# Kernel tuning notes

Hardware: AMD Instinct MI355X
Metric: run time of the kernel (lower is better)

Reference implementation:

```python
import jax, jax.numpy as jnp
import numpy as np

D_MODEL = 1024

def setup_inputs() -> dict:
    key = jax.random.key(0)
    k1, k2 = jax.random.split(key, 2)
    x = jax.random.normal(k1, (4, 2048, D_MODEL), dtype=jnp.float32)
    W_attn = jax.random.normal(k2, (3 * D_MODEL, D_MODEL), dtype=jnp.float32) * (1.0 / np.sqrt(D_MODEL))
    b_attn = jnp.zeros((3 * D_MODEL,), dtype=jnp.float32)
    return {"x": x, "W_attn": W_attn, "b_attn": b_attn}

def reference(x, W_attn, b_attn):
    B, T, C = x.shape
    # fused QKV projection; torch split order is (k, q, v)
    kqv = x @ W_attn.T + b_attn            # [B, T, 3C]
    k, q, v = jnp.split(kqv, 3, axis=-1)   # each [B, T, C]
    # NOTE: original computes k @ q^T (quirk), scaled by sqrt(d_model)
    scores = jnp.einsum('btc,bsc->bts', k, q) / jnp.sqrt(jnp.asarray(C, x.dtype))
    causal = jnp.tril(jnp.ones((T, T), dtype=bool))
    scores = jnp.where(causal[None, :, :], scores, -jnp.inf)
    attn = jax.nn.softmax(scores, axis=-1)
    return jnp.einsum('bts,bsc->btc', attn, v)
```

## Files before the change

kernel.cpp:

```cpp
#include <hip/hip_runtime.h>

typedef __bf16 bf16x8 __attribute__((ext_vector_type(8)));
typedef float f32x4 __attribute__((ext_vector_type(4)));
typedef float fl4 __attribute__((ext_vector_type(4)));
typedef unsigned short us4 __attribute__((ext_vector_type(4)));
typedef unsigned short us8 __attribute__((ext_vector_type(8)));

__device__ __forceinline__ unsigned short f2bf(float f) {
  unsigned u = __builtin_bit_cast(unsigned, f);
  u += 0x7fffu + ((u >> 16) & 1u);
  return (unsigned short)(u >> 16);
}
__device__ __forceinline__ float bf2f(unsigned short h) {
  unsigned u = ((unsigned)h) << 16;
  return __builtin_bit_cast(float, u);
}

__device__ __forceinline__ void async16(const void* g, void* l) {
  __builtin_amdgcn_global_load_lds(
      (const __attribute__((address_space(1))) unsigned int*)g,
      (__attribute__((address_space(3))) unsigned int*)l, 16, 0, 0);
}

#define BARM() asm volatile("s_barrier" ::: "memory")
#define VMCNT4() asm volatile("s_waitcnt vmcnt(4)" ::: "memory")
#define LGKM0() asm volatile("s_waitcnt lgkmcnt(0)" ::: "memory")
#define LGKM8() asm volatile("s_waitcnt lgkmcnt(8)" ::: "memory")
#define SCHEDB() __builtin_amdgcn_sched_barrier(0)

__global__ __launch_bounds__(256) void cvt_bf16_2(const float* __restrict__ sA,
                                                  unsigned short* __restrict__ dA, int nA,
                                                  const float* __restrict__ sB,
                                                  unsigned short* __restrict__ dB, int nB) {
  int i = blockIdx.x * 256 + threadIdx.x;
  const float* s;
  unsigned short* d;
  if (i < nA) {
    s = sA; d = dA;
  } else {
    i -= nA;
    if (i >= nB) return;
    s = sB; d = dB;
  }
  fl4 f = ((const fl4*)s)[i];
  us4 o;
  o[0] = f2bf(f[0]); o[1] = f2bf(f[1]); o[2] = f2bf(f[2]); o[3] = f2bf(f[3]);
  ((us4*)d)[i] = o;
}

__global__ __launch_bounds__(256) void transpose_v(const unsigned short* __restrict__ kqv,
                                                   unsigned short* __restrict__ vT) {
  int b = blockIdx.z;
  int t0 = blockIdx.x * 64;
  int c0 = blockIdx.y * 64;
  __shared__ unsigned short tile[64][68];
  int tid = threadIdx.x;
#pragma unroll
  for (int i = 0; i < 4; ++i) {
    int idx = i * 256 + tid;
    int r = idx >> 4;
    int c4 = (idx & 15) * 4;
    const unsigned short* src = kqv + ((size_t)(b * 2048 + t0 + r)) * 3072 + 2048 + c0 + c4;
    us4 v = *(const us4*)src;
    *(us4*)&tile[r][c4] = v;
  }
  __syncthreads();
#pragma unroll
  for (int i = 0; i < 4; ++i) {
    int idx = i * 256 + tid;
    int rc = idx >> 4;
    int t4 = (idx & 15) * 4;
    us4 v;
    v[0] = tile[t4 + 0][rc]; v[1] = tile[t4 + 1][rc];
    v[2] = tile[t4 + 2][rc]; v[3] = tile[t4 + 3][rc];
    unsigned short* dst = vT + ((size_t)(b * 1024 + c0 + rc)) * 2048 + t0 + t4;
    *(us4*)dst = v;
  }
}

template <int EPI>
__global__ __launch_bounds__(512, 2) void gemm8p(
    const unsigned short* __restrict__ A, int lda, long long sA,
    const unsigned short* __restrict__ B, int ldb, long long sB,
    void* __restrict__ Cv, int ldc, long long sC,
    const float* __restrict__ bias, float scale, int K, int NBX) {
  int bx, by;
  const int bz = blockIdx.z;
  if (EPI == 0) {
    int flat = blockIdx.x;
    int q = (int)gridDim.x >> 3;
    int swz = (flat & 7) * q + (flat >> 3);
    bx = swz % NBX; by = swz / NBX;
  } else {
    bx = blockIdx.x; by = blockIdx.y;
    if (EPI == 1 && bx > by) return;
  }
  A += (size_t)bz * sA;
  B += (size_t)bz * sB;
  const int rowBase = by * 256;
  const int colBase = bx * 256;
  const int nk = (EPI == 2) ? (rowBase + 256) / 64 : K / 64;

  __shared__ __align__(16) unsigned char lds[131072];
  const int tid = threadIdx.x;
  const int lane = tid & 63;
  const int wid = tid >> 6;
  const int wr = wid >> 2;
  const int wc = wid & 3;
  const int l15 = lane & 15, l4 = lane >> 4, l7 = lane & 7;

  f32x4 acc[8][4] = {};
  bf16x8 af0[4][2], af1[4][2], bf0[2][2], bf1[2][2];

  const unsigned short* Ab = A + (size_t)rowBase * lda;
  const unsigned short* Bb = B + (size_t)colBase * ldb;
  unsigned loff[2][2];
  unsigned lldso[2];
#pragma unroll
  for (int i = 0; i < 2; ++i) {
    int off = (i * 512 + tid) * 16;
    int r = off >> 7;
    int sb = ((off >> 4) & 7) ^ (r & 7);
    lldso[i] = (unsigned)off;
#pragma unroll
    for (int h = 0; h < 2; ++h)
      loff[h][i] = (unsigned)((h * 128 + r) * lda + sb * 8);
  }

  auto STAGE = [&](int bufc, int isB, int half, const unsigned short* Gb, int koff) {
#pragma unroll
    for (int i = 0; i < 2; ++i)
      async16(Gb + (size_t)(loff[half][i] + (unsigned)koff),
              lds + bufc * 65536 + isB * 32768 + half * 16384 + lldso[i]);
  };
  auto RDA = [&](int bufc, int m, int kk) -> bf16x8 {
    int row = m * 16 + l15;
    int blk = (kk * 4 + l4) ^ l7;
    return *(const bf16x8*)(lds + bufc * 65536 + wr * 16384 + row * 128 + blk * 16);
  };
  auto RDB = [&](int bufc, int n, int kk) -> bf16x8 {
    int row = (wc & 1) * 64 + n * 16 + l15;
    int blk = (kk * 4 + l4) ^ l7;
    return *(const bf16x8*)(lds + bufc * 65536 + 32768 + (wc >> 1) * 16384 +
                            row * 128 + blk * 16);
  };

#define RDA8(dst, BUF, Q)                                                      \
  _Pragma("unroll") for (int mi = 0; mi < 4; ++mi)                             \
  _Pragma("unroll") for (int kk = 0; kk < 2; ++kk)                             \
      dst[mi][kk] = RDA((BUF), (Q) * 4 + mi, kk)
#define RDB4(dst, BUF, NB)                                                     \
  _Pragma("unroll") for (int nj = 0; nj < 2; ++nj)                             \
  _Pragma("unroll") for (int kk = 0; kk < 2; ++kk)                             \
      dst[nj][kk] = RDB((BUF), (NB) + nj, kk)

#define MFMAQ(MB, NB, AF, BF)                                                  \
  _Pragma("unroll") for (int kk = 0; kk < 2; ++kk)                             \
  _Pragma("unroll") for (int mi = 0; mi < 4; ++mi)                             \
  _Pragma("unroll") for (int nj = 0; nj < 2; ++nj)                             \
      acc[(MB) + mi][(NB) + nj] = __builtin_amdgcn_mfma_f32_16x16x32_bf16(     \
          AF[mi][kk], BF[nj][kk], acc[(MB) + mi][(NB) + nj], 0, 0, 0)

#define PH(RDS, STG, HINT, GATE, MB, NB, AF, BF)                               \
  do {                                                                         \
    RDS;                                                                       \
    STG;                                                                       \
    HINT;                                                                      \
    BARM();                                                                    \
    LGKM0();                                                                   \
    SCHEDB();                                                                  \
    __builtin_amdgcn_s_setprio(1);                                             \
    MFMAQ(MB, NB, AF, BF);                                                     \
    __builtin_amdgcn_s_setprio(0);                                             \
    GATE;                                                                      \
    BARM();                                                                    \
  } while (0)

  STAGE(0, 0, 0, Ab, 0);
  STAGE(0, 0, 1, Ab, 0);
  STAGE(0, 1, 0, Bb, 0);
  STAGE(0, 1, 1, Bb, 0);
  STAGE(1, 1, 0, Bb, 64);
  STAGE(1, 1, 1, Bb, 64);
  VMCNT4();
  BARM();

  const int nt2 = nk >> 1;
  for (int it = 0; it < nt2; ++it) {
    int t = it * 2;
    int kA1 = (t + 1) * 64;
    int k2 = (t + 2 < nk - 1 ? t + 2 : nk - 1) * 64;
    int k3 = (t + 3 < nk - 1 ? t + 3 : nk - 1) * 64;
    PH({ RDA8(af0, 0, 0); RDB4(bf0, 0, 0); }, STAGE(1, 0, 0, Ab, kA1), LGKM8(),
       (void)0, 0, 0, af0, bf0);
    PH({ RDB4(bf1, 0, 2); }, STAGE(1, 0, 1, Ab, kA1), (void)0,
       (void)0, 0, 2, af0, bf1);
    PH({ RDA8(af1, 0, 1); }, STAGE(0, 1, 0, Bb, k2), (void)0,
       (void)0, 4, 2, af1, bf1);
    PH({}, STAGE(0, 1, 1, Bb, k2), (void)0,
       VMCNT4(), 4, 0, af1, bf0);
    PH({ RDA8(af0, 1, 0); RDB4(bf0, 1, 0); }, STAGE(0, 0, 0, Ab, k2), LGKM8(),
       (void)0, 0, 0, af0, bf0);
    PH({ RDB4(bf1, 1, 2); }, STAGE(0, 0, 1, Ab, k2), (void)0,
       (void)0, 0, 2, af0, bf1);
    PH({ RDA8(af1, 1, 1); }, STAGE(1, 1, 0, Bb, k3), (void)0,
       (void)0, 4, 2, af1, bf1);
    PH({}, STAGE(1, 1, 1, Bb, k3), (void)0,
       VMCNT4(), 4, 0, af1, bf0);
  }
#undef PH
#undef MFMAQ
#undef RDA8
#undef RDB4

  const int cr = l4 * 4;
  if constexpr (EPI == 0) {
    unsigned short* C = (unsigned short*)Cv;
#pragma unroll
    for (int n = 0; n < 4; ++n) {
      int col = colBase + wc * 64 + n * 16 + l15;
      float bv = bias[col];
#pragma unroll
      for (int m = 0; m < 8; ++m) {
        int row = rowBase + wr * 128 + m * 16 + cr;
#pragma unroll
        for (int i = 0; i < 4; ++i)
          C[(size_t)(row + i) * ldc + col] = f2bf(acc[m][n][i] + bv);
      }
    }
  } else if constexpr (EPI == 1) {
    unsigned short* C = (unsigned short*)Cv + (size_t)bz * sC;
#pragma unroll
    for (int n = 0; n < 4; ++n) {
      int col = colBase + wc * 64 + n * 16 + l15;
#pragma unroll
      for (int m = 0; m < 8; ++m) {
        int row = rowBase + wr * 128 + m * 16 + cr;
#pragma unroll
        for (int i = 0; i < 4; ++i)
          C[(size_t)(row + i) * ldc + col] = f2bf(acc[m][n][i] * scale);
      }
    }
  } else {
    float* C = (float*)Cv + (size_t)bz * sC;
#pragma unroll
    for (int n = 0; n < 4; ++n) {
      int col = colBase + wc * 64 + n * 16 + l15;
#pragma unroll
      for (int m = 0; m < 8; ++m) {
        int row = rowBase + wr * 128 + m * 16 + cr;
#pragma unroll
        for (int i = 0; i < 4; ++i)
          C[(size_t)(row + i) * ldc + col] = acc[m][n][i];
      }
    }
  }
}

__global__ __launch_bounds__(256) void softmax_causal(unsigned short* __restrict__ S) {
  const int T = 2048;
  int t = blockIdx.x, b = blockIdx.y;
  unsigned short* row = S + ((size_t)b * T + t) * T;
  const int nv = t + 1;
  const int bound = ((t >> 8) + 1) << 8;
  int tid = threadIdx.x;
  int lane = tid & 63, wid = tid >> 6;
  int s0 = tid * 8;
  us8 raw = {};
  if (s0 < nv) raw = *(const us8*)(row + s0);
  float v[8];
  float m = -3.0e38f;
#pragma unroll
  for (int j = 0; j < 8; ++j) {
    v[j] = bf2f(raw[j]);
    if (s0 + j < nv) m = fmaxf(m, v[j]);
  }
#pragma unroll
  for (int o = 32; o > 0; o >>= 1) m = fmaxf(m, __shfl_xor(m, o, 64));
  __shared__ float red[4];
  if (lane == 0) red[wid] = m;
  __syncthreads();
  m = fmaxf(fmaxf(red[0], red[1]), fmaxf(red[2], red[3]));
  __syncthreads();
  float sum = 0.f;
#pragma unroll
  for (int j = 0; j < 8; ++j) {
    float e = (s0 + j < nv) ? exp2f(v[j] - m) : 0.f;
    v[j] = e;
    sum += e;
  }
#pragma unroll
  for (int o = 32; o > 0; o >>= 1) sum += __shfl_xor(sum, o, 64);
  if (lane == 0) red[wid] = sum;
  __syncthreads();
  sum = red[0] + red[1] + red[2] + red[3];
  float inv = 1.0f / sum;
  if (s0 < bound) {
    us8 outv;
#pragma unroll
    for (int j = 0; j < 8; ++j) outv[j] = f2bf(v[j] * inv);
    *(us8*)(row + s0) = outv;
  }
}

extern "C" void kernel_launch(void* const* d_in, const int* in_sizes, int n_in,
                              void* d_out, int out_size, void* d_ws, size_t ws_size,
                              hipStream_t stream) {
  const float* x = (const float*)d_in[0];
  const float* W = (const float*)d_in[1];
  const float* bias = (const float*)d_in[2];
  float* out = (float*)d_out;

  char* ws = (char*)d_ws;
  if (ws_size < 106954752u) return;
  unsigned short* xbf = (unsigned short*)(ws);
  unsigned short* vT = xbf;
  unsigned short* wbf = (unsigned short*)(ws + 16777216);
  unsigned short* kqv = (unsigned short*)(ws + 23068672);
  unsigned short* S = (unsigned short*)(ws + 73400320);

  const float kSoftmaxScale = 1.4426950408889634f / 32.0f;

  cvt_bf16_2<<<11264, 256, 0, stream>>>(x, xbf, 2097152, W, wbf, 786432);

  gemm8p<0><<<dim3(384, 1, 1), 512, 0, stream>>>(
      xbf, 1024, 0LL, wbf, 1024, 0LL, kqv, 3072, 0LL, bias, 1.0f, 1024, 12);

  transpose_v<<<dim3(32, 16, 4), 256, 0, stream>>>(kqv, vT);

  gemm8p<1><<<dim3(8, 8, 4), 512, 0, stream>>>(
      kqv, 3072, 2048LL * 3072, kqv + 1024, 3072, 2048LL * 3072,
      S, 2048, 2048LL * 2048, nullptr, kSoftmaxScale, 1024, 0);

  softmax_causal<<<dim3(2048, 4), 256, 0, stream>>>(S);

  gemm8p<2><<<dim3(4, 8, 4), 512, 0, stream>>>(
      S, 2048, 2048LL * 2048, vT, 2048, 1024LL * 2048,
      out, 1024, 2048LL * 1024, nullptr, 1.0f, 2048, 0);
}
```

Measured before the change: 189.6 us.

## Fuse causal softmax into PV GEMM with online-softmax kernel; change LDS swizzle

Replaces the separate softmax pass and the PV GEMM with one flash-style kernel. It reads the bf16 scaled scores, keeps a running max and sum per row, rescales the accumulators, and multiplies by V with MFMA. This removes a full read-modify-write of the score matrix and one launch. In exchange it uses a small 128x128 tile with a K step of 32 and barriers every step, which may leave the MFMA units poorly fed. The GEMM LDS swizzle is also changed from a per-row XOR to a simpler XOR on bit 2 of the row, which may change bank conflicts.

After: 265.5 us. 1.4x slower.

```diff
diff --git a/kernel.cpp b/kernel.cpp
--- a/kernel.cpp
+++ b/kernel.cpp
@@ -99,7 +99,7 @@
   B += (size_t)bz * sB;
   const int rowBase = by * 256;
   const int colBase = bx * 256;
-  const int nk = (EPI == 2) ? (rowBase + 256) / 64 : K / 64;
+  const int nk = K / 64;
 
   __shared__ __align__(16) unsigned char lds[131072];
   const int tid = threadIdx.x;
@@ -107,7 +107,7 @@
   const int wid = tid >> 6;
   const int wr = wid >> 2;
   const int wc = wid & 3;
-  const int l15 = lane & 15, l4 = lane >> 4, l7 = lane & 7;
+  const int l15 = lane & 15, l4 = lane >> 4;
 
   f32x4 acc[8][4] = {};
   bf16x8 af0[4][2], af1[4][2], bf0[2][2], bf1[2][2];
@@ -120,11 +120,12 @@
   for (int i = 0; i < 2; ++i) {
     int off = (i * 512 + tid) * 16;
     int r = off >> 7;
-    int sb = ((off >> 4) & 7) ^ (r & 7);
+    int c = off & 127;
+    int cs = c ^ (((r >> 2) & 1) << 5);
     lldso[i] = (unsigned)off;
 #pragma unroll
     for (int h = 0; h < 2; ++h)
-      loff[h][i] = (unsigned)((h * 128 + r) * lda + sb * 8);
+      loff[h][i] = (unsigned)((h * 128 + r) * lda + (cs >> 1));
   }
 
   auto STAGE = [&](int bufc, int isB, int half, const unsigned short* Gb, int koff) {
@@ -135,14 +136,14 @@
   };
   auto RDA = [&](int bufc, int m, int kk) -> bf16x8 {
     int row = m * 16 + l15;
-    int blk = (kk * 4 + l4) ^ l7;
-    return *(const bf16x8*)(lds + bufc * 65536 + wr * 16384 + row * 128 + blk * 16);
+    int cs = ((kk * 4 + l4) * 16) ^ (((row >> 2) & 1) << 5);
+    return *(const bf16x8*)(lds + bufc * 65536 + wr * 16384 + row * 128 + cs);
   };
   auto RDB = [&](int bufc, int n, int kk) -> bf16x8 {
     int row = (wc & 1) * 64 + n * 16 + l15;
-    int blk = (kk * 4 + l4) ^ l7;
+    int cs = ((kk * 4 + l4) * 16) ^ (((row >> 2) & 1) << 5);
     return *(const bf16x8*)(lds + bufc * 65536 + 32768 + (wc >> 1) * 16384 +
-                            row * 128 + blk * 16);
+                            row * 128 + cs);
   };
 
 #define RDA8(dst, BUF, Q)                                                      \
@@ -228,7 +229,7 @@
           C[(size_t)(row + i) * ldc + col] = f2bf(acc[m][n][i] + bv);
       }
     }
-  } else if constexpr (EPI == 1) {
+  } else {
     unsigned short* C = (unsigned short*)Cv + (size_t)bz * sC;
 #pragma unroll
     for (int n = 0; n < 4; ++n) {
@@ -241,65 +242,111 @@
           C[(size_t)(row + i) * ldc + col] = f2bf(acc[m][n][i] * scale);
       }
     }
-  } else {
-    float* C = (float*)Cv + (size_t)bz * sC;
-#pragma unroll
-    for (int n = 0; n < 4; ++n) {
-      int col = colBase + wc * 64 + n * 16 + l15;
-#pragma unroll
-      for (int m = 0; m < 8; ++m) {
-        int row = rowBase + wr * 128 + m * 16 + cr;
-#pragma unroll
-        for (int i = 0; i < 4; ++i)
-          C[(size_t)(row + i) * ldc + col] = acc[m][n][i];
-      }
-    }
-  }
-}
-
-__global__ __launch_bounds__(256) void softmax_causal(unsigned short* __restrict__ S) {
-  const int T = 2048;
-  int t = blockIdx.x, b = blockIdx.y;
-  unsigned short* row = S + ((size_t)b * T + t) * T;
-  const int nv = t + 1;
-  const int bound = ((t >> 8) + 1) << 8;
-  int tid = threadIdx.x;
-  int lane = tid & 63, wid = tid >> 6;
-  int s0 = tid * 8;
-  us8 raw = {};
-  if (s0 < nv) raw = *(const us8*)(row + s0);
-  float v[8];
-  float m = -3.0e38f;
-#pragma unroll
-  for (int j = 0; j < 8; ++j) {
-    v[j] = bf2f(raw[j]);
-    if (s0 + j < nv) m = fmaxf(m, v[j]);
-  }
-#pragma unroll
-  for (int o = 32; o > 0; o >>= 1) m = fmaxf(m, __shfl_xor(m, o, 64));
-  __shared__ float red[4];
-  if (lane == 0) red[wid] = m;
-  __syncthreads();
-  m = fmaxf(fmaxf(red[0], red[1]), fmaxf(red[2], red[3]));
-  __syncthreads();
-  float sum = 0.f;
-#pragma unroll
-  for (int j = 0; j < 8; ++j) {
-    float e = (s0 + j < nv) ? exp2f(v[j] - m) : 0.f;
-    v[j] = e;
-    sum += e;
-  }
-#pragma unroll
-  for (int o = 32; o > 0; o >>= 1) sum += __shfl_xor(sum, o, 64);
-  if (lane == 0) red[wid] = sum;
-  __syncthreads();
-  sum = red[0] + red[1] + red[2] + red[3];
-  float inv = 1.0f / sum;
-  if (s0 < bound) {
-    us8 outv;
-#pragma unroll
-    for (int j = 0; j < 8; ++j) outv[j] = f2bf(v[j] * inv);
-    *(us8*)(row + s0) = outv;
+  }
+}
+
+__global__ __launch_bounds__(256, 2) void flash_pv(
+    const unsigned short* __restrict__ S, const unsigned short* __restrict__ V,
+    float* __restrict__ O) {
+  const int bx = blockIdx.x;
+  const int by = (int)gridDim.y - 1 - blockIdx.y;
+  const int bz = blockIdx.z;
+  const unsigned short* Sb = S + (size_t)bz * 2048 * 2048;
+  const unsigned short* Vb = V + (size_t)bz * 1024 * 2048;
+  float* Ob = O + (size_t)bz * 2048 * 1024;
+  const int rowBase = by * 128, colBase = bx * 128;
+  const int nk = (rowBase + 128) / 32;
+
+  __shared__ __align__(16) unsigned char lds[16896];
+  float* scr = (float*)(lds + 16384);
+  const int tid = threadIdx.x;
+  const int lane = tid & 63, wid = tid >> 6;
+  const int l15 = lane & 15, l4 = lane >> 4;
+  const int awrow = wid * 32;
+
+  f32x4 acc[2][8] = {};
+  float mrun[2] = {-3.0e38f, -3.0e38f};
+  float lrun[2] = {0.f, 0.f};
+
+  for (int kt = 0; kt < nk; ++kt) {
+    const int kof = kt * 32;
+    __syncthreads();
+#pragma unroll
+    for (int i = 0; i < 2; ++i) {
+      int off = (i * 256 + tid) * 16;
+      int r = off >> 6;
+      int gblk = ((off >> 4) & 3) ^ ((r >> 1) & 3);
+      async16(Sb + (size_t)(rowBase + r) * 2048 + kof + gblk * 8, lds + off);
+      async16(Vb + (size_t)(colBase + r) * 2048 + kof + gblk * 8, lds + 8192 + off);
+    }
+    __syncthreads();
+    if (kof <= rowBase + awrow + 31) {
+      bf16x8 bfr[8];
+#pragma unroll
+      for (int n = 0; n < 8; ++n) {
+        int row = n * 16 + l15;
+        bfr[n] = *(const bf16x8*)(lds + 8192 + row * 64 + (((l4 ^ (row >> 1)) & 3) * 16));
+      }
+      bf16x8 pa[2];
+#pragma unroll
+      for (int m = 0; m < 2; ++m) {
+        int row = awrow + m * 16 + l15;
+        us8 sraw = *(const us8*)(lds + row * 64 + (((l4 ^ (row >> 1)) & 3) * 16));
+        const int trow = rowBase + row;
+        const int sbase = kof + l4 * 8;
+        float sv[8];
+        float vmax = -3.0e38f;
+#pragma unroll
+        for (int j = 0; j < 8; ++j) {
+          sv[j] = bf2f(sraw[j]);
+          if (sbase + j <= trow) vmax = fmaxf(vmax, sv[j]);
+        }
+        vmax = fmaxf(vmax, __shfl_xor(vmax, 16, 64));
+        vmax = fmaxf(vmax, __shfl_xor(vmax, 32, 64));
+        float mnew = fmaxf(mrun[m], vmax);
+        float sc = exp2f(mrun[m] - mnew);
+        mrun[m] = mnew;
+        float rs = 0.f;
+        us8 pk;
+#pragma unroll
+        for (int j = 0; j < 8; ++j) {
+          float p = (sbase + j <= trow) ? exp2f(sv[j] - mnew) : 0.f;
+          rs += p;
+          pk[j] = f2bf(p);
+        }
+        rs += __shfl_xor(rs, 16, 64);
+        rs += __shfl_xor(rs, 32, 64);
+        lrun[m] = lrun[m] * sc + rs;
+        pa[m] = __builtin_bit_cast(bf16x8, pk);
+        if (l4 == 0) scr[awrow + m * 16 + l15] = sc;
+      }
+#pragma unroll
+      for (int m = 0; m < 2; ++m) {
+#pragma unroll
+        for (int i = 0; i < 4; ++i) {
+          float s = scr[awrow + m * 16 + l4 * 4 + i];
+#pragma unroll
+          for (int n = 0; n < 8; ++n) acc[m][n][i] *= s;
+        }
+#pragma unroll
+        for (int n = 0; n < 8; ++n)
+          acc[m][n] = __builtin_amdgcn_mfma_f32_16x16x32_bf16(pa[m], bfr[n], acc[m][n], 0, 0, 0);
+      }
+    }
+  }
+#pragma unroll
+  for (int m = 0; m < 2; ++m)
+    if (l4 == 0) scr[awrow + m * 16 + l15] = 1.0f / lrun[m];
+#pragma unroll
+  for (int m = 0; m < 2; ++m) {
+#pragma unroll
+    for (int i = 0; i < 4; ++i) {
+      float linv = scr[awrow + m * 16 + l4 * 4 + i];
+      int row = rowBase + awrow + m * 16 + l4 * 4 + i;
+#pragma unroll
+      for (int n = 0; n < 8; ++n)
+        Ob[(size_t)row * 1024 + colBase + n * 16 + l15] = acc[m][n][i] * linv;
+    }
   }
 }
 
@@ -332,9 +379,5 @@
       kqv, 3072, 2048LL * 3072, kqv + 1024, 3072, 2048LL * 3072,
       S, 2048, 2048LL * 2048, nullptr, kSoftmaxScale, 1024, 0);
 
-  softmax_causal<<<dim3(2048, 4), 256, 0, stream>>>(S);
-
-  gemm8p<2><<<dim3(4, 8, 4), 512, 0, stream>>>(
-      S, 2048, 2048LL * 2048, vT, 2048, 1024LL * 2048,
-      out, 1024, 2048LL * 1024, nullptr, 1.0f, 2048, 0);
-}
+  flash_pv<<<dim3(8, 16, 4), 256, 0, stream>>>(S, vT, out);
+}
```

## Add dedicated 128x384-tile QKV projection GEMM kernel with 512-block grid

Applied to the files above, without the earlier changes.

Replaces the generic 256x256-tile gemm8p instantiation for the QKV projection with a specialized kernel using 128x384 tiles. The grid grows from 384 to 512 blocks, which divides evenly across the GPU's compute units and should reduce wave-quantization tail. The kernel keeps the async LDS double-buffered pipeline, with a rebalanced phase schedule and a 4x6 MFMA accumulator layout per wave. In exchange, each tile has a lower compute-to-load ratio, since A and B tiles are less square, and the code carries a second hand-scheduled GEMM to maintain.

After: 184.6 us. 2.6% less time.

```diff
diff --git a/kernel.cpp b/kernel.cpp
--- a/kernel.cpp
+++ b/kernel.cpp
@@ -24,6 +24,7 @@
 
 #define BARM() asm volatile("s_barrier" ::: "memory")
 #define VMCNT4() asm volatile("s_waitcnt vmcnt(4)" ::: "memory")
+#define VMCNT6() asm volatile("s_waitcnt vmcnt(6)" ::: "memory")
 #define LGKM0() asm volatile("s_waitcnt lgkmcnt(0)" ::: "memory")
 #define LGKM8() asm volatile("s_waitcnt lgkmcnt(8)" ::: "memory")
 #define SCHEDB() __builtin_amdgcn_sched_barrier(0)
@@ -78,23 +79,145 @@
   }
 }
 
+__global__ __launch_bounds__(512, 2) void gemm_g0(
+    const unsigned short* __restrict__ A, const unsigned short* __restrict__ B,
+    unsigned short* __restrict__ C, const float* __restrict__ bias) {
+  const int flat = blockIdx.x;
+  const int swz = (flat & 7) * 64 + (flat >> 3);
+  const int bx = swz & 7;
+  const int by = swz >> 3;
+  const int rowBase = by * 128, colBase = bx * 384;
+  const int lda = 1024, ldc = 3072, nk = 16;
+
+  __shared__ __align__(16) unsigned char lds[131072];
+  const int tid = threadIdx.x;
+  const int lane = tid & 63, wid = tid >> 6;
+  const int wr = wid >> 2, wc = wid & 3;
+  const int l15 = lane & 15, l4 = lane >> 4, l7 = lane & 7;
+
+  f32x4 acc[4][6] = {};
+  bf16x8 af01[2][2], af23[2][2], bf[6][2];
+
+  const unsigned short* Ab = A + (size_t)rowBase * lda;
+  const unsigned short* Bb = B + (size_t)colBase * lda;
+  unsigned aoff[2], boff[6], aldso[2], bldso[6];
+#pragma unroll
+  for (int i = 0; i < 6; ++i) {
+    int off = i * 8192 + tid * 16;
+    int r = off >> 7;
+    int sb = ((off >> 4) & 7) ^ (r & 7);
+    if (i < 2) { aoff[i] = (unsigned)(r * lda + sb * 8); aldso[i] = (unsigned)off; }
+    boff[i] = (unsigned)(r * lda + sb * 8);
+    bldso[i] = (unsigned)off;
+  }
+
+  auto STA = [&](int bufc, int op, int koff) {
+    async16(Ab + (size_t)(aoff[op] + (unsigned)koff), lds + bufc * 65536 + aldso[op]);
+  };
+  auto STB = [&](int bufc, int op, int koff) {
+    async16(Bb + (size_t)(boff[op] + (unsigned)koff),
+            lds + bufc * 65536 + 16384 + bldso[op]);
+  };
+  auto RA = [&](int bufc, int m, int kk) -> bf16x8 {
+    int row = wr * 64 + m * 16 + l15;
+    int blk = (kk * 4 + l4) ^ l7;
+    return *(const bf16x8*)(lds + bufc * 65536 + row * 128 + blk * 16);
+  };
+  auto RB = [&](int bufc, int n, int kk) -> bf16x8 {
+    int row = wc * 96 + n * 16 + l15;
+    int blk = (kk * 4 + l4) ^ l7;
+    return *(const bf16x8*)(lds + bufc * 65536 + 16384 + row * 128 + blk * 16);
+  };
+
+#define RD_A01(BUF)                                                            \
+  _Pragma("unroll") for (int mi = 0; mi < 2; ++mi)                             \
+  _Pragma("unroll") for (int kk = 0; kk < 2; ++kk) af01[mi][kk] = RA((BUF), mi, kk)
+#define RD_A23(BUF)                                                            \
+  _Pragma("unroll") for (int mi = 0; mi < 2; ++mi)                             \
+  _Pragma("unroll") for (int kk = 0; kk < 2; ++kk) af23[mi][kk] = RA((BUF), 2 + mi, kk)
+#define RD_B(BUF, N0)                                                          \
+  _Pragma("unroll") for (int nj = 0; nj < 3; ++nj)                             \
+  _Pragma("unroll") for (int kk = 0; kk < 2; ++kk) bf[(N0) + nj][kk] = RB((BUF), (N0) + nj, kk)
+
+#define MQ(MB, NB, AF)                                                         \
+  _Pragma("unroll") for (int kk = 0; kk < 2; ++kk)                             \
+  _Pragma("unroll") for (int mi = 0; mi < 2; ++mi)                             \
+  _Pragma("unroll") for (int nj = 0; nj < 3; ++nj)                             \
+      acc[(MB) + mi][(NB) + nj] = __builtin_amdgcn_mfma_f32_16x16x32_bf16(     \
+          AF[mi][kk], bf[(NB) + nj][kk], acc[(MB) + mi][(NB) + nj], 0, 0, 0)
+
+#define PHASE(RDS, STG, GATE, MB, NB, AF)                                      \
+  do {                                                                         \
+    RDS;                                                                       \
+    STG;                                                                       \
+    BARM();                                                                    \
+    LGKM0();                                                                   \
+    SCHEDB();                                                                  \
+    __builtin_amdgcn_s_setprio(1);                                             \
+    MQ(MB, NB, AF);                                                            \
+    __builtin_amdgcn_s_setprio(0);                                             \
+    GATE;                                                                      \
+    BARM();                                                                    \
+  } while (0)
+
+  STA(0, 0, 0); STA(0, 1, 0);
+#pragma unroll
+  for (int i = 0; i < 6; ++i) STB(0, i, 0);
+#pragma unroll
+  for (int i = 0; i < 6; ++i) STB(1, i, 64);
+  VMCNT6();
+  BARM();
+
+  for (int it = 0; it < 8; ++it) {
+    int t = it * 2;
+    int kA1 = (t + 1) * 64;
+    int k2 = (t + 2 < nk - 1 ? t + 2 : nk - 1) * 64;
+    int k3 = (t + 3 < nk - 1 ? t + 3 : nk - 1) * 64;
+    PHASE({ RD_A01(0); RD_B(0, 0); }, { STA(1, 0, kA1); STA(1, 1, kA1); },
+          (void)0, 0, 0, af01);
+    PHASE({ RD_A23(0); RD_B(0, 3); }, (void)0, (void)0, 0, 3, af01);
+    PHASE({}, { STB(0, 0, k2); STB(0, 1, k2); STB(0, 2, k2); },
+          (void)0, 2, 3, af23);
+    PHASE({}, { STB(0, 3, k2); STB(0, 4, k2); STB(0, 5, k2); },
+          VMCNT6(), 2, 0, af23);
+    PHASE({ RD_A01(1); RD_B(1, 0); }, { STA(0, 0, k2); STA(0, 1, k2); },
+          (void)0, 0, 0, af01);
+    PHASE({ RD_A23(1); RD_B(1, 3); }, (void)0, (void)0, 0, 3, af01);
+    PHASE({}, { STB(1, 0, k3); STB(1, 1, k3); STB(1, 2, k3); },
+          (void)0, 2, 3, af23);
+    PHASE({}, { STB(1, 3, k3); STB(1, 4, k3); STB(1, 5, k3); },
+          VMCNT6(), 2, 0, af23);
+  }
+#undef PHASE
+#undef MQ
+#undef RD_A01
+#undef RD_A23
+#undef RD_B
+
+  const int cr = l4 * 4;
+#pragma unroll
+  for (int n = 0; n < 6; ++n) {
+    int col = colBase + wc * 96 + n * 16 + l15;
+    float bv = bias[col];
+#pragma unroll
+    for (int m = 0; m < 4; ++m) {
+      int row = rowBase + wr * 64 + m * 16 + cr;
+#pragma unroll
+      for (int i = 0; i < 4; ++i)
+        C[(size_t)(row + i) * ldc + col] = f2bf(acc[m][n][i] + bv);
+    }
+  }
+}
+
 template <int EPI>
 __global__ __launch_bounds__(512, 2) void gemm8p(
     const unsigned short* __restrict__ A, int lda, long long sA,
     const unsigned short* __restrict__ B, int ldb, long long sB,
     void* __restrict__ Cv, int ldc, long long sC,
-    const float* __restrict__ bias, float scale, int K, int NBX) {
-  int bx, by;
+    float scale, int K) {
+  int bx = blockIdx.x, by = blockIdx.y;
   const int bz = blockIdx.z;
-  if (EPI == 0) {
-    int flat = blockIdx.x;
-    int q = (int)gridDim.x >> 3;
-    int swz = (flat & 7) * q + (flat >> 3);
-    bx = swz % NBX; by = swz / NBX;
-  } else {
-    bx = blockIdx.x; by = blockIdx.y;
-    if (EPI == 1 && bx > by) return;
-  }
+  if (EPI == 1 && bx > by) return;
   A += (size_t)bz * sA;
   B += (size_t)bz * sB;
   const int rowBase = by * 256;
@@ -180,8 +303,11 @@
   STAGE(0, 0, 1, Ab, 0);
   STAGE(0, 1, 0, Bb, 0);
   STAGE(0, 1, 1, Bb, 0);
-  STAGE(1, 1, 0, Bb, 64);
-  STAGE(1, 1, 1, Bb, 64);
+  {
+    int k1 = ((1 < nk - 1) ? 1 : (nk - 1)) * 64;
+    STAGE(1, 1, 0, Bb, k1);
+    STAGE(1, 1, 1, Bb, k1);
+  }
   VMCNT4();
   BARM();
 
@@ -214,21 +340,7 @@
 #undef RDB4
 
   const int cr = l4 * 4;
-  if constexpr (EPI == 0) {
-    unsigned short* C = (unsigned short*)Cv;
-#pragma unroll
-    for (int n = 0; n < 4; ++n) {
-      int col = colBase + wc * 64 + n * 16 + l15;
-      float bv = bias[col];
-#pragma unroll
-      for (int m = 0; m < 8; ++m) {
-        int row = rowBase + wr * 128 + m * 16 + cr;
-#pragma unroll
-        for (int i = 0; i < 4; ++i)
-          C[(size_t)(row + i) * ldc + col] = f2bf(acc[m][n][i] + bv);
-      }
-    }
-  } else if constexpr (EPI == 1) {
+  if constexpr (EPI == 1) {
     unsigned short* C = (unsigned short*)Cv + (size_t)bz * sC;
 #pragma unroll
     for (int n = 0; n < 4; ++n) {
@@ -323,18 +435,17 @@
 
   cvt_bf16_2<<<11264, 256, 0, stream>>>(x, xbf, 2097152, W, wbf, 786432);
 
-  gemm8p<0><<<dim3(384, 1, 1), 512, 0, stream>>>(
-      xbf, 1024, 0LL, wbf, 1024, 0LL, kqv, 3072, 0LL, bias, 1.0f, 1024, 12);
+  gemm_g0<<<dim3(512, 1, 1), 512, 0, stream>>>(xbf, wbf, kqv, bias);
 
   transpose_v<<<dim3(32, 16, 4), 256, 0, stream>>>(kqv, vT);
 
   gemm8p<1><<<dim3(8, 8, 4), 512, 0, stream>>>(
       kqv, 3072, 2048LL * 3072, kqv + 1024, 3072, 2048LL * 3072,
-      S, 2048, 2048LL * 2048, nullptr, kSoftmaxScale, 1024, 0);
+      S, 2048, 2048LL * 2048, kSoftmaxScale, 1024);
 
   softmax_causal<<<dim3(2048, 4), 256, 0, stream>>>(S);
 
   gemm8p<2><<<dim3(4, 8, 4), 512, 0, stream>>>(
       S, 2048, 2048LL * 2048, vT, 2048, 1024LL * 2048,
-      out, 1024, 2048LL * 1024, nullptr, 1.0f, 2048, 0);
-}
+      out, 1024, 2048LL * 1024, 1.0f, 2048);
+}
```
